# Kernel optimization log

Hardware: AMD Instinct MI355X
Metric: run time of the kernel (lower is better)

## Reference

```python
import jax, jax.numpy as jnp
import numpy as np

NEG_BIG = -1e30  # safe "-inf" for masked softmax (avoids NaN for fully-masked rows)


def setup_inputs() -> dict:
    key = jax.random.key(0)
    k1, k2, k3, k4, k5, k6 = jax.random.split(key, 6)
    B, Kmax, D, C = 64, 512, 256, 1000
    deep_feats = jax.random.normal(k1, (B, D), dtype=jnp.float32)
    n = jax.random.normal(k2, (B, Kmax, D), dtype=jnp.float32)
    w = jax.random.uniform(k3, (B, Kmax), dtype=jnp.float32)
    cls_score = jax.random.normal(k4, (B, Kmax, C), dtype=jnp.float32)
    target = jax.random.randint(k5, (B,), 0, C, dtype=jnp.int64)
    lengths = jax.random.randint(k6, (B,), 1, Kmax + 1, dtype=jnp.int64)
    return {"deep_feats": deep_feats, "n": n, "w": w, "cls_score": cls_score,
            "target": target, "lengths": lengths}


def reference(deep_feats, n, w, cls_score, target, lengths):
    # deep_feats: [B,D], n: [B,Kmax,D], w: [B,Kmax], cls_score: [B,Kmax,C]
    # target: [B] int, lengths: [B] int (number of valid neighbors per sample)
    B, Kmax, C = cls_score.shape
    mask = jnp.arange(Kmax)[None, :] < lengths[:, None]          # [B,Kmax]

    # per-neighbor L2 distance ||f_i - n_ij||
    diff = deep_feats[:, None, :] - n                             # [B,Kmax,D]
    dist = jnp.sqrt(jnp.sum(diff * diff, axis=-1))                # [B,Kmax]

    s = -w * dist                                                 # [B,Kmax]
    # f_loss = sum_i -w_i . dist_i over valid neighbors
    f_loss = jnp.sum(jnp.where(mask, s, 0.0))

    # rho_i = softmax over valid neighbors of -w*dist
    logits = jnp.where(mask, s, NEG_BIG)
    rho = jax.nn.softmax(logits, axis=-1) * mask                  # [B,Kmax]

    # per-neighbor cross-entropy: -log_softmax(cls_score[b,k])[target[b]]
    logp = jax.nn.log_softmax(cls_score, axis=-1)                 # [B,Kmax,C]
    idx = jnp.broadcast_to(target[:, None, None], (B, Kmax, 1))
    ce = -jnp.take_along_axis(logp, idx, axis=-1)[..., 0]         # [B,Kmax]

    g_loss = jnp.sum(rho * ce)
    return f_loss + g_loss
```

## Files before the change

kernel.cpp:

```cpp
#include <hip/hip_runtime.h>
#include <math.h>

#define BB 64
#define KMAX 512
#define DD 256
#define CC 1000

__device__ __forceinline__ float wave_reduce_sum(float v) {
    #pragma unroll
    for (int off = 32; off > 0; off >>= 1) v += __shfl_xor(v, off, 64);
    return v;
}

__global__ void __launch_bounds__(256)
dos_row_kernel(const float* __restrict__ deep, const float* __restrict__ n,
               const float* __restrict__ w, const float* __restrict__ cls,
               const int* __restrict__ target, const int* __restrict__ lengths,
               float* __restrict__ s_out, float* __restrict__ ce_out,
               float* __restrict__ out) {
    const int wid  = threadIdx.x >> 6;
    const int lane = threadIdx.x & 63;
    const int row  = blockIdx.x * 4 + wid;
    const int b    = row >> 9;
    const int k    = row & (KMAX - 1);

    if (blockIdx.x == 0 && threadIdx.x == 0) out[0] = 0.f;

    if (k >= lengths[b]) return;

    const float4 dv = ((const float4*)(deep + (size_t)b * DD))[lane];
    const float4 nv = ((const float4*)(n + (size_t)row * DD))[lane];
    const float* __restrict__ x = cls + (size_t)row * CC;
    const float4 v0 = ((const float4*)x)[lane];
    const float4 v1 = ((const float4*)x)[lane + 64];
    const float4 v2 = ((const float4*)x)[lane + 128];
    float4 v3 = make_float4(-1e30f, -1e30f, -1e30f, -1e30f);
    if (lane < 58) v3 = ((const float4*)x)[lane + 192];

    const float dx = dv.x - nv.x, dy = dv.y - nv.y;
    const float dz = dv.z - nv.z, dw = dv.w - nv.w;
    float acc = dx*dx + dy*dy + dz*dz + dw*dw;
    acc = wave_reduce_sum(acc);

    float e = __expf(v0.x) + __expf(v0.y) + __expf(v0.z) + __expf(v0.w)
            + __expf(v1.x) + __expf(v1.y) + __expf(v1.z) + __expf(v1.w)
            + __expf(v2.x) + __expf(v2.y) + __expf(v2.z) + __expf(v2.w)
            + __expf(v3.x) + __expf(v3.y) + __expf(v3.z) + __expf(v3.w);
    e = wave_reduce_sum(e);

    if (lane == 0) {
        s_out[row]  = -w[row] * sqrtf(acc);
        ce_out[row] = __logf(e) - x[target[b]];
    }
}

__global__ void __launch_bounds__(512)
dos_combine_kernel(const float* __restrict__ s, const float* __restrict__ ce,
                   const int* __restrict__ lengths, float* __restrict__ out) {
    const int b = blockIdx.x;
    const int k = threadIdx.x;
    const bool valid = k < lengths[b];

    const float sv = s[b * KMAX + k];
    const float cv = ce[b * KMAX + k];

    float e  = valid ? __expf(sv) : 0.f;
    float fs = valid ? sv : 0.f;
    float ec = valid ? e * cv : 0.f;

    e  = wave_reduce_sum(e);
    fs = wave_reduce_sum(fs);
    ec = wave_reduce_sum(ec);

    __shared__ float r1[8], r2[8], r3[8];
    if ((k & 63) == 0) { r1[k >> 6] = e; r2[k >> 6] = fs; r3[k >> 6] = ec; }
    __syncthreads();
    if (k == 0) {
        float se = 0.f, sf = 0.f, sc = 0.f;
        #pragma unroll
        for (int i = 0; i < 8; i++) { se += r1[i]; sf += r2[i]; sc += r3[i]; }
        atomicAdd(out, sf + sc / se);
    }
}

extern "C" void kernel_launch(void* const* d_in, const int* in_sizes, int n_in,
                              void* d_out, int out_size, void* d_ws, size_t ws_size,
                              hipStream_t stream) {
    const float* deep    = (const float*)d_in[0];
    const float* n       = (const float*)d_in[1];
    const float* w       = (const float*)d_in[2];
    const float* cls     = (const float*)d_in[3];
    const int*   target  = (const int*)d_in[4];
    const int*   lengths = (const int*)d_in[5];
    float*       out     = (float*)d_out;

    float* ws = (float*)d_ws;
    float* s  = ws;
    float* ce = ws + BB * KMAX;

    dos_row_kernel<<<(BB * KMAX) / 4, 256, 0, stream>>>(deep, n, w, cls, target,
                                                        lengths, s, ce, out);
    dos_combine_kernel<<<BB, KMAX, 0, stream>>>(s, ce, lengths, out);
}
```

Measured before the change: 22.51 us.

## Accumulate per-batch softmax sums with atomics and replace combine kernel

Each wave now computes exp(s) and exp(s)*ce itself and atomically adds s, exp(s) and exp(s)*ce into four striped slots per batch, instead of writing s and ce to workspace for a 512-thread combine kernel. A tiny single-wave final kernel sums the slots and forms f_loss plus g_loss. It relies on the s values being non-positive so that exp(s) needs no max subtraction, and it adds a memset plus contended float atomics, which make the result order-nondeterministic.

```diff
diff --git a/kernel.cpp b/kernel.cpp
--- a/kernel.cpp
+++ b/kernel.cpp
@@ -5,6 +5,7 @@
 #define KMAX 512
 #define DD 256
 #define CC 1000
+#define NSLOT 4
 
 __device__ __forceinline__ float wave_reduce_sum(float v) {
     #pragma unroll
@@ -16,15 +17,13 @@
 dos_row_kernel(const float* __restrict__ deep, const float* __restrict__ n,
                const float* __restrict__ w, const float* __restrict__ cls,
                const int* __restrict__ target, const int* __restrict__ lengths,
-               float* __restrict__ s_out, float* __restrict__ ce_out,
-               float* __restrict__ out) {
+               float* __restrict__ accS, float* __restrict__ accE,
+               float* __restrict__ accEC) {
     const int wid  = threadIdx.x >> 6;
     const int lane = threadIdx.x & 63;
     const int row  = blockIdx.x * 4 + wid;
     const int b    = row >> 9;
     const int k    = row & (KMAX - 1);
-
-    if (blockIdx.x == 0 && threadIdx.x == 0) out[0] = 0.f;
 
     if (k >= lengths[b]) return;
 
@@ -49,38 +48,30 @@
     e = wave_reduce_sum(e);
 
     if (lane == 0) {
-        s_out[row]  = -w[row] * sqrtf(acc);
-        ce_out[row] = __logf(e) - x[target[b]];
+        const float sv  = -w[row] * sqrtf(acc);
+        const float cev = __logf(e) - x[target[b]];
+        const float ev  = __expf(sv);
+        const int slot  = (b << 2) + (k & (NSLOT - 1));
+        atomicAdd(&accS[slot],  sv);
+        atomicAdd(&accE[slot],  ev);
+        atomicAdd(&accEC[slot], ev * cev);
     }
 }
 
-__global__ void __launch_bounds__(512)
-dos_combine_kernel(const float* __restrict__ s, const float* __restrict__ ce,
-                   const int* __restrict__ lengths, float* __restrict__ out) {
-    const int b = blockIdx.x;
-    const int k = threadIdx.x;
-    const bool valid = k < lengths[b];
-
-    const float sv = s[b * KMAX + k];
-    const float cv = ce[b * KMAX + k];
-
-    float e  = valid ? __expf(sv) : 0.f;
-    float fs = valid ? sv : 0.f;
-    float ec = valid ? e * cv : 0.f;
-
-    e  = wave_reduce_sum(e);
-    fs = wave_reduce_sum(fs);
-    ec = wave_reduce_sum(ec);
-
-    __shared__ float r1[8], r2[8], r3[8];
-    if ((k & 63) == 0) { r1[k >> 6] = e; r2[k >> 6] = fs; r3[k >> 6] = ec; }
-    __syncthreads();
-    if (k == 0) {
-        float se = 0.f, sf = 0.f, sc = 0.f;
-        #pragma unroll
-        for (int i = 0; i < 8; i++) { se += r1[i]; sf += r2[i]; sc += r3[i]; }
-        atomicAdd(out, sf + sc / se);
-    }
+__global__ void dos_final_kernel(const float4* __restrict__ accS4,
+                                 const float4* __restrict__ accE4,
+                                 const float4* __restrict__ accEC4,
+                                 float* __restrict__ out) {
+    const int b = threadIdx.x;
+    const float4 s4  = accS4[b];
+    const float4 e4  = accE4[b];
+    const float4 ec4 = accEC4[b];
+    const float sS  = s4.x + s4.y + s4.z + s4.w;
+    const float sE  = e4.x + e4.y + e4.z + e4.w;
+    const float sEC = ec4.x + ec4.y + ec4.z + ec4.w;
+    float v = sS + sEC / sE;
+    v = wave_reduce_sum(v);
+    if (b == 0) out[0] = v;
 }
 
 extern "C" void kernel_launch(void* const* d_in, const int* in_sizes, int n_in,
@@ -94,11 +85,14 @@
     const int*   lengths = (const int*)d_in[5];
     float*       out     = (float*)d_out;
 
-    float* ws = (float*)d_ws;
-    float* s  = ws;
-    float* ce = ws + BB * KMAX;
+    float* ws    = (float*)d_ws;
+    float* accS  = ws;
+    float* accE  = ws + BB * NSLOT;
+    float* accEC = ws + 2 * BB * NSLOT;
 
+    hipMemsetAsync(ws, 0, 3 * BB * NSLOT * sizeof(float), stream);
     dos_row_kernel<<<(BB * KMAX) / 4, 256, 0, stream>>>(deep, n, w, cls, target,
-                                                        lengths, s, ce, out);
-    dos_combine_kernel<<<BB, KMAX, 0, stream>>>(s, ce, lengths, out);
+                                                        lengths, accS, accE, accEC);
+    dos_final_kernel<<<1, 64, 0, stream>>>((const float4*)accS, (const float4*)accE,
+                                           (const float4*)accEC, out);
 }
```

After: 64.62 us. 2.87x slower.
